# Performance work log

Measured on AMD Instinct MI355X. Metric: run time of the kernel, lower is better.

Reference implementation:

```python
import jax, jax.numpy as jnp
import numpy as np

B, S, E = 4, 2048, 2048
QH, KH = 16, 4
HD = E // QH            # 128 head dim
KVE = HD * KH           # 512 kv embed dim
LN_EPS = 1e-5


def act_quant(x):
    # BitNet 1.58: per-token 8-bit absmax activation quantization
    scale = 127.0 / jnp.clip(jnp.max(jnp.abs(x), axis=-1, keepdims=True), 1e-5)
    return jnp.clip(jnp.round(x * scale), -128.0, 127.0) / scale


def weight_quant(w):
    # BitNet 1.58: ternary {-1,0,1} weight quantization via mean-abs scale
    scale = 1.0 / jnp.clip(jnp.mean(jnp.abs(w)), 1e-5)
    return jnp.clip(jnp.round(w * scale), -1.0, 1.0) / scale


def bitlinear(x, w, b):
    # straight-through estimator form: quantized forward, identity backward
    xq = x + jax.lax.stop_gradient(act_quant(x) - x)
    wq = w + jax.lax.stop_gradient(weight_quant(w) - w)
    return xq @ wq.T + b


def setup_inputs() -> dict:
    ks = jax.random.split(jax.random.key(0), 16)
    w = lambda k, shp: jax.random.normal(k, shp, jnp.float32) * 0.02
    return {
        "query": jax.random.normal(ks[0], (B, S, E), jnp.float32),
        "key":   jax.random.normal(ks[1], (B, S, E), jnp.float32),
        "value": jax.random.normal(ks[2], (B, S, E), jnp.float32),
        "Wq": w(ks[3], (E, E)),   "bq": jnp.zeros((E,),   jnp.float32),
        "Wk": w(ks[4], (KVE, E)), "bk": jnp.zeros((KVE,), jnp.float32),
        "Wv": w(ks[5], (KVE, E)), "bv": jnp.zeros((KVE,), jnp.float32),
        "Wo": w(ks[6], (E, KVE)), "bo": jnp.zeros((E,),   jnp.float32),
        "gamma": jnp.ones((KVE,), jnp.float32),
        "beta":  jnp.zeros((KVE,), jnp.float32),
    }


def reference(query, key, value, Wq, bq, Wk, bk, Wv, bv, Wo, bo, gamma, beta):
    q = bitlinear(query, Wq, bq)   # [B,N,E]
    k = bitlinear(key,   Wk, bk)   # [B,S,KVE]
    v = bitlinear(value, Wv, bv)   # [B,S,KVE]
    b_, n = q.shape[0], q.shape[1]
    s = k.shape[1]
    q = q.reshape(b_, n, QH, HD)
    k = k.reshape(b_, s, KH, HD)
    v = v.reshape(b_, s, KH, HD)
    scale = float(HD) ** 0.5
    # b h n d with query heads split into (kv_head, group); group axis is SUMMED
    # (faithful to the source einsum 'b g h n d, b h s d -> b h n s')
    qh = (q / scale).transpose(0, 2, 1, 3).reshape(b_, KH, QH // KH, n, HD)
    kh = k.transpose(0, 2, 1, 3)   # [B,KH,S,HD]
    vh = v.transpose(0, 2, 1, 3)   # [B,KH,S,HD]
    sim = jnp.einsum('bhgnd,bhsd->bhns', qh, kh)
    mask = jnp.tril(jnp.ones((n, s), dtype=bool))
    sim = jnp.where(mask, sim, jnp.finfo(sim.dtype).min)
    # note: source divides by scale twice (q/scale then sim/scale)
    attn = jax.nn.softmax(sim / scale, axis=-1)
    out = jnp.einsum('bhns,bhsd->bhnd', attn, vh)
    x = out.transpose(0, 2, 1, 3).reshape(b_, n, KVE)
    mu = jnp.mean(x, axis=-1, keepdims=True)
    var = jnp.var(x, axis=-1, keepdims=True)
    x = (x - mu) / jnp.sqrt(var + LN_EPS) * gamma + beta
    return bitlinear(x, Wo, bo)
```

## Files before the change

### kernel.cpp

```cpp
#include <hip/hip_runtime.h>
#include <hip/hip_fp16.h>

typedef _Float16 f16;
typedef __attribute__((ext_vector_type(8))) _Float16 f16x8;
typedef __attribute__((ext_vector_type(4))) _Float16 f16x4;
typedef __attribute__((ext_vector_type(2))) _Float16 f16x2;
typedef __attribute__((ext_vector_type(4))) float f32x4;

#define AS1(p) ((__attribute__((address_space(1))) char*)(p))
#define AS3(p) ((__attribute__((address_space(3))) char*)(p))

static __device__ __forceinline__ float wave_red_sum(float v) {
#pragma unroll
  for (int m = 1; m < 64; m <<= 1) v += __shfl_xor(v, m);
  return v;
}
static __device__ __forceinline__ float wave_red_max(float v) {
#pragma unroll
  for (int m = 1; m < 64; m <<= 1) v = fmaxf(v, __shfl_xor(v, m));
  return v;
}

__global__ __launch_bounds__(256) void absum_partial(
    const float* __restrict__ Wq, const float* __restrict__ Wk,
    const float* __restrict__ Wv, const float* __restrict__ Wo,
    float* __restrict__ partial) {
  const int w = blockIdx.x >> 8;
  const int lb = blockIdx.x & 255;
  const float* W = (w == 0) ? Wq : (w == 1) ? Wk : (w == 2) ? Wv : Wo;
  const int per_block = (w == 0) ? (4194304 >> 8) : (1048576 >> 8);
  const float* base = W + (size_t)lb * per_block;
  float s = 0.f;
  for (int i = threadIdx.x * 4; i < per_block; i += 256 * 4) {
    float4 v = *(const float4*)(base + i);
    s += fabsf(v.x) + fabsf(v.y) + fabsf(v.z) + fabsf(v.w);
  }
  s = wave_red_sum(s);
  __shared__ float red[4];
  const int wave = threadIdx.x >> 6, lane = threadIdx.x & 63;
  if (lane == 0) red[wave] = s;
  __syncthreads();
  if (threadIdx.x == 0) partial[blockIdx.x] = red[0] + red[1] + red[2] + red[3];
}

__global__ __launch_bounds__(256) void absum_final(const float* __restrict__ partial,
                                                   float* __restrict__ scales) {
  const int wave = threadIdx.x >> 6, lane = threadIdx.x & 63;
  const float* p = partial + wave * 256;
  float s = p[lane] + p[lane + 64] + p[lane + 128] + p[lane + 192];
  s = wave_red_sum(s);
  if (lane == 0) {
    const float cnt = (wave == 0) ? 4194304.f : 1048576.f;
    const float mean = s / cnt;
    const float mul = 1.0f / fmaxf(mean, 1e-5f);
    scales[wave] = mul;
    scales[4 + wave] = 1.0f / mul;
  }
}

__global__ __launch_bounds__(256) void quant_w_ternary(const float* __restrict__ W,
                                                       f16* __restrict__ W8,
                                                       const float* __restrict__ scales,
                                                       int widx, int n) {
  const float mul = scales[widx];
  const int i = (blockIdx.x * 256 + threadIdx.x) * 4;
  if (i >= n) return;
  float4 v = *(const float4*)(W + i);
  f16x4 o;
  o[0] = (f16)fminf(fmaxf(rintf(v.x * mul), -1.f), 1.f);
  o[1] = (f16)fminf(fmaxf(rintf(v.y * mul), -1.f), 1.f);
  o[2] = (f16)fminf(fmaxf(rintf(v.z * mul), -1.f), 1.f);
  o[3] = (f16)fminf(fmaxf(rintf(v.w * mul), -1.f), 1.f);
  *(f16x4*)(W8 + i) = o;
}

__global__ __launch_bounds__(256) void quant_wq_eff(const float* __restrict__ Wq,
                                                    f16* __restrict__ We,
                                                    const float* __restrict__ scales) {
  const float mul = scales[0];
  const int idx = (blockIdx.x * 256 + threadIdx.x) * 4;
  const int j = idx >> 11, e = idx & 2047;
  const int h = j >> 7, d = j & 127;
  float a0 = 0, a1 = 0, a2 = 0, a3 = 0;
#pragma unroll
  for (int g = 0; g < 4; g++) {
    const float* src = Wq + (size_t)((h * 4 + g) * 128 + d) * 2048 + e;
    float4 v = *(const float4*)src;
    a0 += fminf(fmaxf(rintf(v.x * mul), -1.f), 1.f);
    a1 += fminf(fmaxf(rintf(v.y * mul), -1.f), 1.f);
    a2 += fminf(fmaxf(rintf(v.z * mul), -1.f), 1.f);
    a3 += fminf(fmaxf(rintf(v.w * mul), -1.f), 1.f);
  }
  f16x4 o; o[0] = (f16)a0; o[1] = (f16)a1; o[2] = (f16)a2; o[3] = (f16)a3;
  *(f16x4*)(We + idx) = o;
}

__global__ void bq_eff_kernel(const float* __restrict__ bq, float* __restrict__ be) {
  const int j = blockIdx.x * 256 + threadIdx.x;
  if (j >= 512) return;
  const int h = j >> 7, d = j & 127;
  float s = 0.f;
#pragma unroll
  for (int g = 0; g < 4; g++) s += bq[(h * 4 + g) * 128 + d];
  be[j] = s;
}

__global__ __launch_bounds__(256) void quant_act3(
    const float* __restrict__ Xq, const float* __restrict__ Xk, const float* __restrict__ Xv,
    f16* __restrict__ Aq, f16* __restrict__ Ak, f16* __restrict__ Av,
    float* __restrict__ deq3) {
  const int which = blockIdx.y;
  const float* X = which == 0 ? Xq : which == 1 ? Xk : Xv;
  f16* Q = which == 0 ? Aq : which == 1 ? Ak : Av;
  float* deq = deq3 + which * 8192;
  const size_t tok = blockIdx.x;
  const float* x = X + tok * 2048;
  const int t = threadIdx.x;
  float4 v0 = *(const float4*)(x + t * 8);
  float4 v1 = *(const float4*)(x + t * 8 + 4);
  float amax = fmaxf(fmaxf(fmaxf(fabsf(v0.x), fabsf(v0.y)), fmaxf(fabsf(v0.z), fabsf(v0.w))),
                     fmaxf(fmaxf(fabsf(v1.x), fabsf(v1.y)), fmaxf(fabsf(v1.z), fabsf(v1.w))));
  amax = wave_red_max(amax);
  __shared__ float red[4];
  const int wave = t >> 6, lane = t & 63;
  if (lane == 0) red[wave] = amax;
  __syncthreads();
  amax = fmaxf(fmaxf(red[0], red[1]), fmaxf(red[2], red[3]));
  const float scale = 127.0f / fmaxf(amax, 1e-5f);
  f16x8 q;
  q[0] = (f16)fminf(fmaxf(rintf(v0.x * scale), -128.f), 127.f);
  q[1] = (f16)fminf(fmaxf(rintf(v0.y * scale), -128.f), 127.f);
  q[2] = (f16)fminf(fmaxf(rintf(v0.z * scale), -128.f), 127.f);
  q[3] = (f16)fminf(fmaxf(rintf(v0.w * scale), -128.f), 127.f);
  q[4] = (f16)fminf(fmaxf(rintf(v1.x * scale), -128.f), 127.f);
  q[5] = (f16)fminf(fmaxf(rintf(v1.y * scale), -128.f), 127.f);
  q[6] = (f16)fminf(fmaxf(rintf(v1.z * scale), -128.f), 127.f);
  q[7] = (f16)fminf(fmaxf(rintf(v1.w * scale), -128.f), 127.f);
  *(f16x8*)(Q + tok * 2048 + t * 8) = q;
  if (t == 0) deq[tok] = 1.0f / scale;
}

template <typename OutT>
static __device__ __forceinline__ void gemm_core(
    const f16* __restrict__ A, const f16* __restrict__ W,
    const float* __restrict__ deqA, const float dW,
    const float* __restrict__ bias, OutT* __restrict__ C,
    const int N, const int K, const float out_scale, const int bm, const int bn,
    f16* __restrict__ As, f16* __restrict__ Bs) {
  const int t = threadIdx.x;
  const int wave = t >> 6, lane = t & 63;
  const int lg = lane >> 4, ln = lane & 15;
  const int wr = (wave >> 1) * 64, wc = (wave & 1) * 64;
  f32x4 acc[4][4] = {};
  const f16* gA = A + (size_t)(bm * 128 + (t >> 2)) * K + (t & 3) * 8;
  const f16* gB = W + (size_t)(bn * 128 + (t >> 2)) * K + (t & 3) * 8;
  const int wb = wave * 1024;

  for (int k0 = 0; k0 < K; k0 += 32) {
    __builtin_amdgcn_global_load_lds(AS1(gA + k0), AS3((char*)As + wb), 16, 0, 0);
    __builtin_amdgcn_global_load_lds(AS1(gA + (size_t)64 * K + k0), AS3((char*)As + 4096 + wb), 16, 0, 0);
    __builtin_amdgcn_global_load_lds(AS1(gB + k0), AS3((char*)Bs + wb), 16, 0, 0);
    __builtin_amdgcn_global_load_lds(AS1(gB + (size_t)64 * K + k0), AS3((char*)Bs + 4096 + wb), 16, 0, 0);
    __syncthreads();
    f16x8 af[4], bf[4];
#pragma unroll
    for (int fr = 0; fr < 4; fr++) af[fr] = *(const f16x8*)(As + (wr + fr * 16 + ln) * 32 + lg * 8);
#pragma unroll
    for (int fc = 0; fc < 4; fc++) bf[fc] = *(const f16x8*)(Bs + (wc + fc * 16 + ln) * 32 + lg * 8);
    __builtin_amdgcn_s_setprio(1);
#pragma unroll
    for (int fr = 0; fr < 4; fr++)
#pragma unroll
      for (int fc = 0; fc < 4; fc++)
        acc[fr][fc] = __builtin_amdgcn_mfma_f32_16x16x32_f16(af[fr], bf[fc], acc[fr][fc], 0, 0, 0);
    __builtin_amdgcn_s_setprio(0);
    __syncthreads();
  }
#pragma unroll
  for (int fr = 0; fr < 4; fr++) {
#pragma unroll
    for (int r = 0; r < 4; r++) {
      const int grow = bm * 128 + wr + fr * 16 + lg * 4 + r;
      const float dA = deqA[grow] * dW;
#pragma unroll
      for (int fc = 0; fc < 4; fc++) {
        const int gcol = bn * 128 + wc + fc * 16 + ln;
        const float y = (acc[fr][fc][r] * dA + bias[gcol]) * out_scale;
        C[(size_t)grow * N + gcol] = (OutT)y;
      }
    }
  }
}

__global__ __launch_bounds__(256) void gemm_qkv(
    const f16* __restrict__ Aq, const f16* __restrict__ Ak, const f16* __restrict__ Av,
    const f16* __restrict__ Wqe, const f16* __restrict__ Wk8, const f16* __restrict__ Wv8,
    const float* __restrict__ deq3, const float* __restrict__ scales,
    const float* __restrict__ bqe, const float* __restrict__ bk, const float* __restrict__ bv,
    f16* __restrict__ Cq, f16* __restrict__ Ck, f16* __restrict__ Cv) {
  __shared__ f16 As[128 * 32];
  __shared__ f16 Bs[128 * 32];
  const int orig = blockIdx.x + (blockIdx.y << 2) + (blockIdx.z << 8);
  const int wk = ((orig & 7) * 96) + (orig >> 3);
  const int z = wk >> 8, rem = wk & 255, bm = rem >> 2, bn = rem & 3;
  const f16* A = z == 0 ? Aq : z == 1 ? Ak : Av;
  const f16* W = z == 0 ? Wqe : z == 1 ? Wk8 : Wv8;
  const float* bias = z == 0 ? bqe : z == 1 ? bk : bv;
  f16* C = z == 0 ? Cq : z == 1 ? Ck : Cv;
  gemm_core<f16>(A, W, deq3 + z * 8192, scales[4 + z], bias, C,
                 512, 2048, z == 0 ? (1.0f / 128.0f) : 1.0f, bm, bn, As, Bs);
}

__global__ __launch_bounds__(256) void gemm_o(
    const f16* __restrict__ A, const f16* __restrict__ W,
    const float* __restrict__ deqA, const float* __restrict__ scales,
    const float* __restrict__ bias, float* __restrict__ C) {
  __shared__ f16 As[128 * 32];
  __shared__ f16 Bs[128 * 32];
  const int orig = blockIdx.x + (blockIdx.y << 4);
  const int wk = ((orig & 7) * 128) + (orig >> 3);
  const int bm = wk >> 4, bn = wk & 15;
  gemm_core<float>(A, W, deqA, scales[7], bias, C, 2048, 512, 1.0f, bm, bn, As, Bs);
}

static __device__ __forceinline__ void stage_k(char* ksb, const f16* src, int wave) {
#pragma unroll
  for (int i = 0; i < 4; i++)
    __builtin_amdgcn_global_load_lds(AS1(src + (size_t)i * 16 * 512),
                                     AS3(ksb + i * 4096 + wave * 1024), 16, 0, 0);
}

static __device__ __forceinline__ void write_v(f16* vsb, int vsp, int vdp,
                                               f16x8 va0, f16x8 va1, f16x8 vb0, f16x8 vb1) {
#pragma unroll
  for (int j = 0; j < 8; j++) {
    const int d0 = vdp + j;
    const int m0 = ((d0 ^ (d0 >> 4)) & 7) << 3;
    f16x2 p0; p0[0] = va0[j]; p0[1] = vb0[j];
    *(f16x2*)(vsb + d0 * 64 + (vsp ^ m0)) = p0;
    const int d1 = vdp + 8 + j;
    const int m1 = ((d1 ^ (d1 >> 4)) & 7) << 3;
    f16x2 p1; p1[0] = va1[j]; p1[1] = vb1[j];
    *(f16x2*)(vsb + d1 * 64 + (vsp ^ m1)) = p1;
  }
}

__global__ __launch_bounds__(256) void attn_kernel(
    const f16* __restrict__ Qs, const f16* __restrict__ Kq, const f16* __restrict__ Vq,
    float* __restrict__ X) {
  __shared__ f16 Ks[2][64 * 128];
  __shared__ f16 Vs[2][128 * 64];
  __shared__ f16 Ps[4][16 * 72];
  const int pr = blockIdx.x, bh = blockIdx.y;
  const int b = bh >> 2, h = bh & 3;
  const int t = threadIdx.x, wave = t >> 6, lane = t & 63;
  const int lg = lane >> 4, ln = lane & 15;
  const size_t base = (size_t)b * 2048 * 512 + h * 128;

  const int krow16 = wave * 4 + (lane >> 4);
  const int kcol = ((lane & 15) * 8) ^ ((krow16 & 7) << 3);
  const f16* gK0 = Kq + base + (size_t)krow16 * 512 + kcol;
  const int vsp = (t >> 3) * 2, vdp = (t & 7) * 16;
  const f16* gV0 = Vq + base + (size_t)vsp * 512 + vdp;

  for (int pass = 0; pass < 2; ++pass) {
    const int qt = pass ? (31 - pr) : pr;
    const int nt = qt + 1;
    f16x8 qf[4];
    {
      const int qrow = qt * 64 + wave * 16 + ln;
      const f16* qp = Qs + base + (size_t)qrow * 512 + lg * 8;
#pragma unroll
      for (int ks = 0; ks < 4; ks++) qf[ks] = *(const f16x8*)(qp + ks * 32);
    }
    f32x4 o[8] = {};
    float m_r[4], l_r[4];
#pragma unroll
    for (int r = 0; r < 4; r++) { m_r[r] = -1e30f; l_r[r] = 0.f; }

    f16x8 va0, va1, vb0, vb1;
    stage_k((char*)&Ks[0][0], gK0, wave);
    {
      const f16* gv = gV0;
      va0 = *(const f16x8*)(gv);       va1 = *(const f16x8*)(gv + 8);
      vb0 = *(const f16x8*)(gv + 512); vb1 = *(const f16x8*)(gv + 520);
    }
    write_v(&Vs[0][0], vsp, vdp, va0, va1, vb0, vb1);
    __syncthreads();

    for (int ti = 0; ti < nt; ++ti) {
      const int buf = ti & 1, nbuf = buf ^ 1;
      const bool pf = (ti + 1 < nt);
      if (pf) {
        stage_k((char*)&Ks[nbuf][0], gK0 + (size_t)(ti + 1) * 64 * 512, wave);
        const f16* gv = gV0 + (size_t)(ti + 1) * 64 * 512;
        va0 = *(const f16x8*)(gv);       va1 = *(const f16x8*)(gv + 8);
        vb0 = *(const f16x8*)(gv + 512); vb1 = *(const f16x8*)(gv + 520);
      }
      const int s0 = ti * 64;
      f32x4 sacc[4] = {};
      __builtin_amdgcn_s_setprio(1);
#pragma unroll
      for (int ks = 0; ks < 4; ks++)
#pragma unroll
        for (int fc = 0; fc < 4; fc++) {
          const int row = fc * 16 + ln;
          f16x8 bf = *(const f16x8*)(&Ks[buf][row * 128 + ((ks * 32 + lg * 8) ^ ((ln & 7) << 3))]);
          sacc[fc] = __builtin_amdgcn_mfma_f32_16x16x32_f16(qf[ks], bf, sacc[fc], 0, 0, 0);
        }
      __builtin_amdgcn_s_setprio(0);
      if (ti == nt - 1) {
        const int rbase = qt * 64 + wave * 16 + lg * 4;
#pragma unroll
        for (int fc = 0; fc < 4; fc++) {
          const int col = s0 + fc * 16 + ln;
#pragma unroll
          for (int r = 0; r < 4; r++)
            if (col > rbase + r) sacc[fc][r] = -1e30f;
        }
      }
      float tm[4];
#pragma unroll
      for (int r = 0; r < 4; r++)
        tm[r] = fmaxf(fmaxf(sacc[0][r], sacc[1][r]), fmaxf(sacc[2][r], sacc[3][r]));
#pragma unroll
      for (int r = 0; r < 4; r++) {
#pragma unroll
        for (int msk = 1; msk < 16; msk <<= 1) tm[r] = fmaxf(tm[r], __shfl_xor(tm[r], msk));
      }
      float al[4], ps[4];
#pragma unroll
      for (int r = 0; r < 4; r++) {
        const float mn = fmaxf(m_r[r], tm[r]);
        al[r] = __expf(m_r[r] - mn);
        m_r[r] = mn;
        ps[r] = 0.f;
      }
#pragma unroll
      for (int fc = 0; fc < 4; fc++)
#pragma unroll
        for (int r = 0; r < 4; r++) {
          const float p = __expf(sacc[fc][r] - m_r[r]);
          ps[r] += p;
          Ps[wave][(lg * 4 + r) * 72 + fc * 16 + ln] = (f16)p;
        }
#pragma unroll
      for (int r = 0; r < 4; r++) {
#pragma unroll
        for (int msk = 1; msk < 16; msk <<= 1) ps[r] += __shfl_xor(ps[r], msk);
        l_r[r] = l_r[r] * al[r] + ps[r];
      }
#pragma unroll
      for (int fc2 = 0; fc2 < 8; fc2++)
#pragma unroll
        for (int r = 0; r < 4; r++) o[fc2][r] *= al[r];
      __builtin_amdgcn_s_setprio(1);
#pragma unroll
      for (int ks2 = 0; ks2 < 2; ks2++) {
        f16x8 pa = *(const f16x8*)(&Ps[wave][ln * 72 + ks2 * 32 + lg * 8]);
#pragma unroll
        for (int fc2 = 0; fc2 < 8; fc2++) {
          const int d = fc2 * 16 + ln;
          f16x8 vbf = *(const f16x8*)(&Vs[buf][d * 64 +
                          ((ks2 * 32 + lg * 8) ^ (((ln ^ fc2) & 7) << 3))]);
          o[fc2] = __builtin_amdgcn_mfma_f32_16x16x32_f16(pa, vbf, o[fc2], 0, 0, 0);
        }
      }
      __builtin_amdgcn_s_setprio(0);
      if (pf) write_v(&Vs[nbuf][0], vsp, vdp, va0, va1, vb0, vb1);
      __syncthreads();
    }
    const int rbase = qt * 64 + wave * 16 + lg * 4;
#pragma unroll
    for (int r = 0; r < 4; r++) {
      const float inv = 1.0f / l_r[r];
      float* xp = X + ((size_t)b * 2048 + rbase + r) * 512 + h * 128 + ln;
#pragma unroll
      for (int fc2 = 0; fc2 < 8; fc2++) xp[fc2 * 16] = o[fc2][r] * inv;
    }
  }
}

__global__ __launch_bounds__(256) void ln_quant(const float* __restrict__ X,
                                                const float* __restrict__ gamma,
                                                const float* __restrict__ beta,
                                                f16* __restrict__ Q, float* __restrict__ deq) {
  const size_t tok = blockIdx.x;
  const int t = threadIdx.x;
  const float* x = X + tok * 512;
  float2 v = *(const float2*)(x + t * 2);
  float s = v.x + v.y, sq = v.x * v.x + v.y * v.y;
  s = wave_red_sum(s);
  sq = wave_red_sum(sq);
  __shared__ float rs[4], rq[4], rm[4];
  const int wave = t >> 6, lane = t & 63;
  if (lane == 0) { rs[wave] = s; rq[wave] = sq; }
  __syncthreads();
  s = rs[0] + rs[1] + rs[2] + rs[3];
  sq = rq[0] + rq[1] + rq[2] + rq[3];
  const float mean = s * (1.0f / 512.0f);
  const float var = sq * (1.0f / 512.0f) - mean * mean;
  const float inv = 1.0f / sqrtf(var + 1e-5f);
  float2 g = *(const float2*)(gamma + t * 2);
  float2 be = *(const float2*)(beta + t * 2);
  const float t0 = (v.x - mean) * inv * g.x + be.x;
  const float t1 = (v.y - mean) * inv * g.y + be.y;
  float amax = fmaxf(fabsf(t0), fabsf(t1));
  amax = wave_red_max(amax);
  if (lane == 0) rm[wave] = amax;
  __syncthreads();
  amax = fmaxf(fmaxf(rm[0], rm[1]), fmaxf(rm[2], rm[3]));
  const float scale = 127.0f / fmaxf(amax, 1e-5f);
  f16x2 q;
  q[0] = (f16)fminf(fmaxf(rintf(t0 * scale), -128.f), 127.f);
  q[1] = (f16)fminf(fmaxf(rintf(t1 * scale), -128.f), 127.f);
  *(f16x2*)(Q + tok * 512 + t * 2) = q;
  if (t == 0) deq[tok] = 1.0f / scale;
}

extern "C" void kernel_launch(void* const* d_in, const int* in_sizes, int n_in,
                              void* d_out, int out_size, void* d_ws, size_t ws_size,
                              hipStream_t stream) {
  const float* query = (const float*)d_in[0];
  const float* key   = (const float*)d_in[1];
  const float* value = (const float*)d_in[2];
  const float* Wq = (const float*)d_in[3];
  const float* bq = (const float*)d_in[4];
  const float* Wk = (const float*)d_in[5];
  const float* bk = (const float*)d_in[6];
  const float* Wv = (const float*)d_in[7];
  const float* bv = (const float*)d_in[8];
  const float* Wo = (const float*)d_in[9];
  const float* bo = (const float*)d_in[10];
  const float* gamma = (const float*)d_in[11];
  const float* beta  = (const float*)d_in[12];

  char* ws = (char*)d_ws;
  size_t off = 0;
  auto alloc = [&](size_t bytes) {
    char* p = ws + off;
    off = (off + bytes + 255) & ~(size_t)255;
    return p;
  };
  float* partial = (float*)alloc(1024 * 4);
  float* scales  = (float*)alloc(8 * 4);
  float* bqe     = (float*)alloc(512 * 4);
  f16* Wqe = (f16*)alloc((size_t)512 * 2048 * 2);
  f16* Wk8 = (f16*)alloc((size_t)512 * 2048 * 2);
  f16* Wv8 = (f16*)alloc((size_t)512 * 2048 * 2);
  f16* Wo8 = (f16*)alloc((size_t)2048 * 512 * 2);
  f16* a8v = (f16*)alloc((size_t)8192 * 2048 * 2);
  float* deq3 = (float*)alloc(3 * 8192 * 4);
  float* deqO = (float*)alloc(8192 * 4);
  f16* qs = (f16*)alloc((size_t)8192 * 512 * 2);
  f16* kq = (f16*)alloc((size_t)8192 * 512 * 2);
  f16* vq = (f16*)alloc((size_t)8192 * 512 * 2);
  float* x = (float*)alloc((size_t)8192 * 512 * 4);
  f16* a8o = (f16*)alloc((size_t)8192 * 512 * 2);
  (void)ws_size; (void)in_sizes; (void)n_in; (void)out_size;

  f16* a8q = (f16*)d_out;
  f16* a8k = (f16*)d_out + (size_t)8192 * 2048;

  absum_partial<<<1024, 256, 0, stream>>>(Wq, Wk, Wv, Wo, partial);
  absum_final<<<1, 256, 0, stream>>>(partial, scales);
  quant_wq_eff<<<1024, 256, 0, stream>>>(Wq, Wqe, scales);
  bq_eff_kernel<<<2, 256, 0, stream>>>(bq, bqe);
  quant_w_ternary<<<1024, 256, 0, stream>>>(Wk, Wk8, scales, 1, 1048576);
  quant_w_ternary<<<1024, 256, 0, stream>>>(Wv, Wv8, scales, 2, 1048576);
  quant_w_ternary<<<1024, 256, 0, stream>>>(Wo, Wo8, scales, 3, 1048576);

  quant_act3<<<dim3(8192, 3), 256, 0, stream>>>(query, key, value, a8q, a8k, a8v, deq3);
  gemm_qkv<<<dim3(4, 64, 3), 256, 0, stream>>>(a8q, a8k, a8v, Wqe, Wk8, Wv8, deq3, scales,
                                               bqe, bk, bv, qs, kq, vq);

  attn_kernel<<<dim3(16, 16), 256, 0, stream>>>(qs, kq, vq, x);

  ln_quant<<<8192, 256, 0, stream>>>(x, gamma, beta, a8o, deqO);
  gemm_o<<<dim3(16, 64), 256, 0, stream>>>(a8o, Wo8, deqO, scales, bo, (float*)d_out);
}
```

Measured before the change: 484.4 us.

## Switch bitlinear GEMMs to int8 MFMA with double-buffered swizzled LDS

```diff
diff --git a/kernel.cpp b/kernel.cpp
--- a/kernel.cpp
+++ b/kernel.cpp
@@ -6,6 +6,7 @@
 typedef __attribute__((ext_vector_type(4))) _Float16 f16x4;
 typedef __attribute__((ext_vector_type(2))) _Float16 f16x2;
 typedef __attribute__((ext_vector_type(4))) float f32x4;
+typedef __attribute__((ext_vector_type(4))) int i32x4;
 
 #define AS1(p) ((__attribute__((address_space(1))) char*)(p))
 #define AS3(p) ((__attribute__((address_space(3))) char*)(p))
@@ -19,6 +20,9 @@
 #pragma unroll
   for (int m = 1; m < 64; m <<= 1) v = fmaxf(v, __shfl_xor(v, m));
   return v;
+}
+static __device__ __forceinline__ int pack4(int q0, int q1, int q2, int q3) {
+  return (q0 & 255) | ((q1 & 255) << 8) | ((q2 & 255) << 16) | ((q3 & 255) << 24);
 }
 
 __global__ __launch_bounds__(256) void absum_partial(
@@ -58,24 +62,33 @@
   }
 }
 
-__global__ __launch_bounds__(256) void quant_w_ternary(const float* __restrict__ W,
-                                                       f16* __restrict__ W8,
-                                                       const float* __restrict__ scales,
-                                                       int widx, int n) {
-  const float mul = scales[widx];
-  const int i = (blockIdx.x * 256 + threadIdx.x) * 4;
-  if (i >= n) return;
-  float4 v = *(const float4*)(W + i);
-  f16x4 o;
-  o[0] = (f16)fminf(fmaxf(rintf(v.x * mul), -1.f), 1.f);
-  o[1] = (f16)fminf(fmaxf(rintf(v.y * mul), -1.f), 1.f);
-  o[2] = (f16)fminf(fmaxf(rintf(v.z * mul), -1.f), 1.f);
-  o[3] = (f16)fminf(fmaxf(rintf(v.w * mul), -1.f), 1.f);
-  *(f16x4*)(W8 + i) = o;
+__global__ __launch_bounds__(256) void quant_w3(
+    const float* __restrict__ Wk, const float* __restrict__ Wv, const float* __restrict__ Wo,
+    char* __restrict__ Ok, char* __restrict__ Ov, char* __restrict__ Oo,
+    const float* __restrict__ scales) {
+  const int z = blockIdx.y;
+  const float* W = z == 0 ? Wk : z == 1 ? Wv : Wo;
+  char* O = z == 0 ? Ok : z == 1 ? Ov : Oo;
+  const float mul = scales[1 + z];
+  const int i = (blockIdx.x * 256 + threadIdx.x) * 8;
+  float4 a = *(const float4*)(W + i);
+  float4 b = *(const float4*)(W + i + 4);
+  const int q0 = (int)fminf(fmaxf(rintf(a.x * mul), -1.f), 1.f);
+  const int q1 = (int)fminf(fmaxf(rintf(a.y * mul), -1.f), 1.f);
+  const int q2 = (int)fminf(fmaxf(rintf(a.z * mul), -1.f), 1.f);
+  const int q3 = (int)fminf(fmaxf(rintf(a.w * mul), -1.f), 1.f);
+  const int q4 = (int)fminf(fmaxf(rintf(b.x * mul), -1.f), 1.f);
+  const int q5 = (int)fminf(fmaxf(rintf(b.y * mul), -1.f), 1.f);
+  const int q6 = (int)fminf(fmaxf(rintf(b.z * mul), -1.f), 1.f);
+  const int q7 = (int)fminf(fmaxf(rintf(b.w * mul), -1.f), 1.f);
+  int2 p;
+  p.x = pack4(q0, q1, q2, q3);
+  p.y = pack4(q4, q5, q6, q7);
+  *(int2*)(O + i) = p;
 }
 
 __global__ __launch_bounds__(256) void quant_wq_eff(const float* __restrict__ Wq,
-                                                    f16* __restrict__ We,
+                                                    char* __restrict__ We,
                                                     const float* __restrict__ scales) {
   const float mul = scales[0];
   const int idx = (blockIdx.x * 256 + threadIdx.x) * 4;
@@ -91,8 +104,7 @@
     a2 += fminf(fmaxf(rintf(v.z * mul), -1.f), 1.f);
     a3 += fminf(fmaxf(rintf(v.w * mul), -1.f), 1.f);
   }
-  f16x4 o; o[0] = (f16)a0; o[1] = (f16)a1; o[2] = (f16)a2; o[3] = (f16)a3;
-  *(f16x4*)(We + idx) = o;
+  *(int*)(We + idx) = pack4((int)a0, (int)a1, (int)a2, (int)a3);
 }
 
 __global__ void bq_eff_kernel(const float* __restrict__ bq, float* __restrict__ be) {
@@ -107,11 +119,11 @@
 
 __global__ __launch_bounds__(256) void quant_act3(
     const float* __restrict__ Xq, const float* __restrict__ Xk, const float* __restrict__ Xv,
-    f16* __restrict__ Aq, f16* __restrict__ Ak, f16* __restrict__ Av,
+    char* __restrict__ Aq, char* __restrict__ Ak, char* __restrict__ Av,
     float* __restrict__ deq3) {
   const int which = blockIdx.y;
   const float* X = which == 0 ? Xq : which == 1 ? Xk : Xv;
-  f16* Q = which == 0 ? Aq : which == 1 ? Ak : Av;
+  char* Q = which == 0 ? Aq : which == 1 ? Ak : Av;
   float* deq = deq3 + which * 8192;
   const size_t tok = blockIdx.x;
   const float* x = X + tok * 2048;
@@ -127,54 +139,69 @@
   __syncthreads();
   amax = fmaxf(fmaxf(red[0], red[1]), fmaxf(red[2], red[3]));
   const float scale = 127.0f / fmaxf(amax, 1e-5f);
-  f16x8 q;
-  q[0] = (f16)fminf(fmaxf(rintf(v0.x * scale), -128.f), 127.f);
-  q[1] = (f16)fminf(fmaxf(rintf(v0.y * scale), -128.f), 127.f);
-  q[2] = (f16)fminf(fmaxf(rintf(v0.z * scale), -128.f), 127.f);
-  q[3] = (f16)fminf(fmaxf(rintf(v0.w * scale), -128.f), 127.f);
-  q[4] = (f16)fminf(fmaxf(rintf(v1.x * scale), -128.f), 127.f);
-  q[5] = (f16)fminf(fmaxf(rintf(v1.y * scale), -128.f), 127.f);
-  q[6] = (f16)fminf(fmaxf(rintf(v1.z * scale), -128.f), 127.f);
-  q[7] = (f16)fminf(fmaxf(rintf(v1.w * scale), -128.f), 127.f);
-  *(f16x8*)(Q + tok * 2048 + t * 8) = q;
+  const int q0 = (int)fminf(fmaxf(rintf(v0.x * scale), -128.f), 127.f);
+  const int q1 = (int)fminf(fmaxf(rintf(v0.y * scale), -128.f), 127.f);
+  const int q2 = (int)fminf(fmaxf(rintf(v0.z * scale), -128.f), 127.f);
+  const int q3 = (int)fminf(fmaxf(rintf(v0.w * scale), -128.f), 127.f);
+  const int q4 = (int)fminf(fmaxf(rintf(v1.x * scale), -128.f), 127.f);
+  const int q5 = (int)fminf(fmaxf(rintf(v1.y * scale), -128.f), 127.f);
+  const int q6 = (int)fminf(fmaxf(rintf(v1.z * scale), -128.f), 127.f);
+  const int q7 = (int)fminf(fmaxf(rintf(v1.w * scale), -128.f), 127.f);
+  int2 p;
+  p.x = pack4(q0, q1, q2, q3);
+  p.y = pack4(q4, q5, q6, q7);
+  *(int2*)(Q + tok * 2048 + t * 8) = p;
   if (t == 0) deq[tok] = 1.0f / scale;
 }
 
+static __device__ __forceinline__ void stage_i8(const char* src, char* dst, int wave, int K) {
+  __builtin_amdgcn_global_load_lds(AS1(src), AS3(dst + wave * 1024), 16, 0, 0);
+  __builtin_amdgcn_global_load_lds(AS1(src + (size_t)64 * K), AS3(dst + 4096 + wave * 1024), 16, 0, 0);
+}
+
 template <typename OutT>
-static __device__ __forceinline__ void gemm_core(
-    const f16* __restrict__ A, const f16* __restrict__ W,
+static __device__ __forceinline__ void gemm_core_i8(
+    const char* __restrict__ A, const char* __restrict__ W,
     const float* __restrict__ deqA, const float dW,
     const float* __restrict__ bias, OutT* __restrict__ C,
     const int N, const int K, const float out_scale, const int bm, const int bn,
-    f16* __restrict__ As, f16* __restrict__ Bs) {
+    char* As, char* Bs) {
   const int t = threadIdx.x;
   const int wave = t >> 6, lane = t & 63;
   const int lg = lane >> 4, ln = lane & 15;
   const int wr = (wave >> 1) * 64, wc = (wave & 1) * 64;
-  f32x4 acc[4][4] = {};
-  const f16* gA = A + (size_t)(bm * 128 + (t >> 2)) * K + (t & 3) * 8;
-  const f16* gB = W + (size_t)(bn * 128 + (t >> 2)) * K + (t & 3) * 8;
-  const int wb = wave * 1024;
-
-  for (int k0 = 0; k0 < K; k0 += 32) {
-    __builtin_amdgcn_global_load_lds(AS1(gA + k0), AS3((char*)As + wb), 16, 0, 0);
-    __builtin_amdgcn_global_load_lds(AS1(gA + (size_t)64 * K + k0), AS3((char*)As + 4096 + wb), 16, 0, 0);
-    __builtin_amdgcn_global_load_lds(AS1(gB + k0), AS3((char*)Bs + wb), 16, 0, 0);
-    __builtin_amdgcn_global_load_lds(AS1(gB + (size_t)64 * K + k0), AS3((char*)Bs + 4096 + wb), 16, 0, 0);
-    __syncthreads();
-    f16x8 af[4], bf[4];
-#pragma unroll
-    for (int fr = 0; fr < 4; fr++) af[fr] = *(const f16x8*)(As + (wr + fr * 16 + ln) * 32 + lg * 8);
-#pragma unroll
-    for (int fc = 0; fc < 4; fc++) bf[fc] = *(const f16x8*)(Bs + (wc + fc * 16 + ln) * 32 + lg * 8);
+  i32x4 acc[4][4] = {};
+  const int swS = ((t & 3) ^ ((t >> 3) & 3)) * 16;
+  const char* gA = A + (size_t)(bm * 128 + (t >> 2)) * K + swS;
+  const char* gB = W + (size_t)(bn * 128 + (t >> 2)) * K + swS;
+  const int swR = (lg ^ ((ln >> 1) & 3)) * 16;
+  const int NI = K >> 6;
+
+  stage_i8(gA, As, wave, K);
+  stage_i8(gB, Bs, wave, K);
+  __syncthreads();
+  int buf = 0;
+  for (int it = 0; it < NI; ++it) {
+    if (it + 1 < NI) {
+      stage_i8(gA + (it + 1) * 64, As + ((buf ^ 1) << 13), wave, K);
+      stage_i8(gB + (it + 1) * 64, Bs + ((buf ^ 1) << 13), wave, K);
+    }
+    i32x4 af[4], bf[4];
+#pragma unroll
+    for (int fr = 0; fr < 4; fr++)
+      af[fr] = *(const i32x4*)(As + (buf << 13) + (wr + fr * 16 + ln) * 64 + swR);
+#pragma unroll
+    for (int fc = 0; fc < 4; fc++)
+      bf[fc] = *(const i32x4*)(Bs + (buf << 13) + (wc + fc * 16 + ln) * 64 + swR);
     __builtin_amdgcn_s_setprio(1);
 #pragma unroll
     for (int fr = 0; fr < 4; fr++)
 #pragma unroll
       for (int fc = 0; fc < 4; fc++)
-        acc[fr][fc] = __builtin_amdgcn_mfma_f32_16x16x32_f16(af[fr], bf[fc], acc[fr][fc], 0, 0, 0);
+        acc[fr][fc] = __builtin_amdgcn_mfma_i32_16x16x64_i8(af[fr], bf[fc], acc[fr][fc], 0, 0, 0);
     __builtin_amdgcn_s_setprio(0);
     __syncthreads();
+    buf ^= 1;
   }
 #pragma unroll
   for (int fr = 0; fr < 4; fr++) {
@@ -185,42 +212,42 @@
 #pragma unroll
       for (int fc = 0; fc < 4; fc++) {
         const int gcol = bn * 128 + wc + fc * 16 + ln;
-        const float y = (acc[fr][fc][r] * dA + bias[gcol]) * out_scale;
-        C[(size_t)grow * N + gcol] = (OutT)y;
+        C[(size_t)grow * N + gcol] = (OutT)(((float)acc[fr][fc][r] * dA + bias[gcol]) * out_scale);
       }
     }
   }
 }
 
 __global__ __launch_bounds__(256) void gemm_qkv(
-    const f16* __restrict__ Aq, const f16* __restrict__ Ak, const f16* __restrict__ Av,
-    const f16* __restrict__ Wqe, const f16* __restrict__ Wk8, const f16* __restrict__ Wv8,
+    const char* __restrict__ Aq, const char* __restrict__ Ak, const char* __restrict__ Av,
+    const char* __restrict__ Wqe, const char* __restrict__ Wk8, const char* __restrict__ Wv8,
     const float* __restrict__ deq3, const float* __restrict__ scales,
     const float* __restrict__ bqe, const float* __restrict__ bk, const float* __restrict__ bv,
     f16* __restrict__ Cq, f16* __restrict__ Ck, f16* __restrict__ Cv) {
-  __shared__ f16 As[128 * 32];
-  __shared__ f16 Bs[128 * 32];
+  __shared__ __align__(16) char As[2][8192];
+  __shared__ __align__(16) char Bs[2][8192];
   const int orig = blockIdx.x + (blockIdx.y << 2) + (blockIdx.z << 8);
   const int wk = ((orig & 7) * 96) + (orig >> 3);
   const int z = wk >> 8, rem = wk & 255, bm = rem >> 2, bn = rem & 3;
-  const f16* A = z == 0 ? Aq : z == 1 ? Ak : Av;
-  const f16* W = z == 0 ? Wqe : z == 1 ? Wk8 : Wv8;
+  const char* A = z == 0 ? Aq : z == 1 ? Ak : Av;
+  const char* W = z == 0 ? Wqe : z == 1 ? Wk8 : Wv8;
   const float* bias = z == 0 ? bqe : z == 1 ? bk : bv;
   f16* C = z == 0 ? Cq : z == 1 ? Ck : Cv;
-  gemm_core<f16>(A, W, deq3 + z * 8192, scales[4 + z], bias, C,
-                 512, 2048, z == 0 ? (1.0f / 128.0f) : 1.0f, bm, bn, As, Bs);
+  gemm_core_i8<f16>(A, W, deq3 + z * 8192, scales[4 + z], bias, C,
+                    512, 2048, z == 0 ? (1.0f / 128.0f) : 1.0f, bm, bn, &As[0][0], &Bs[0][0]);
 }
 
 __global__ __launch_bounds__(256) void gemm_o(
-    const f16* __restrict__ A, const f16* __restrict__ W,
+    const char* __restrict__ A, const char* __restrict__ W,
     const float* __restrict__ deqA, const float* __restrict__ scales,
     const float* __restrict__ bias, float* __restrict__ C) {
-  __shared__ f16 As[128 * 32];
-  __shared__ f16 Bs[128 * 32];
+  __shared__ __align__(16) char As[2][8192];
+  __shared__ __align__(16) char Bs[2][8192];
   const int orig = blockIdx.x + (blockIdx.y << 4);
   const int wk = ((orig & 7) * 128) + (orig >> 3);
   const int bm = wk >> 4, bn = wk & 15;
-  gemm_core<float>(A, W, deqA, scales[7], bias, C, 2048, 512, 1.0f, bm, bn, As, Bs);
+  gemm_core_i8<float>(A, W, deqA, scales[7], bias, C, 2048, 512, 1.0f, bm, bn,
+                      &As[0][0], &Bs[0][0]);
 }
 
 static __device__ __forceinline__ void stage_k(char* ksb, const f16* src, int wave) {
@@ -384,7 +411,7 @@
 __global__ __launch_bounds__(256) void ln_quant(const float* __restrict__ X,
                                                 const float* __restrict__ gamma,
                                                 const float* __restrict__ beta,
-                                                f16* __restrict__ Q, float* __restrict__ deq) {
+                                                char* __restrict__ Q, float* __restrict__ deq) {
   const size_t tok = blockIdx.x;
   const int t = threadIdx.x;
   const float* x = X + tok * 512;
@@ -411,10 +438,9 @@
   __syncthreads();
   amax = fmaxf(fmaxf(rm[0], rm[1]), fmaxf(rm[2], rm[3]));
   const float scale = 127.0f / fmaxf(amax, 1e-5f);
-  f16x2 q;
-  q[0] = (f16)fminf(fmaxf(rintf(t0 * scale), -128.f), 127.f);
-  q[1] = (f16)fminf(fmaxf(rintf(t1 * scale), -128.f), 127.f);
-  *(f16x2*)(Q + tok * 512 + t * 2) = q;
+  const int q0 = (int)fminf(fmaxf(rintf(t0 * scale), -128.f), 127.f);
+  const int q1 = (int)fminf(fmaxf(rintf(t1 * scale), -128.f), 127.f);
+  *(unsigned short*)(Q + tok * 512 + t * 2) = (unsigned short)((q0 & 255) | ((q1 & 255) << 8));
   if (t == 0) deq[tok] = 1.0f / scale;
 }
 
@@ -445,30 +471,28 @@
   float* partial = (float*)alloc(1024 * 4);
   float* scales  = (float*)alloc(8 * 4);
   float* bqe     = (float*)alloc(512 * 4);
-  f16* Wqe = (f16*)alloc((size_t)512 * 2048 * 2);
-  f16* Wk8 = (f16*)alloc((size_t)512 * 2048 * 2);
-  f16* Wv8 = (f16*)alloc((size_t)512 * 2048 * 2);
-  f16* Wo8 = (f16*)alloc((size_t)2048 * 512 * 2);
-  f16* a8v = (f16*)alloc((size_t)8192 * 2048 * 2);
+  char* Wqe = alloc((size_t)512 * 2048);
+  char* Wk8 = alloc((size_t)512 * 2048);
+  char* Wv8 = alloc((size_t)512 * 2048);
+  char* Wo8 = alloc((size_t)2048 * 512);
+  char* a8v = alloc((size_t)8192 * 2048);
   float* deq3 = (float*)alloc(3 * 8192 * 4);
   float* deqO = (float*)alloc(8192 * 4);
   f16* qs = (f16*)alloc((size_t)8192 * 512 * 2);
   f16* kq = (f16*)alloc((size_t)8192 * 512 * 2);
   f16* vq = (f16*)alloc((size_t)8192 * 512 * 2);
   float* x = (float*)alloc((size_t)8192 * 512 * 4);
-  f16* a8o = (f16*)alloc((size_t)8192 * 512 * 2);
+  char* a8o = alloc((size_t)8192 * 512);
   (void)ws_size; (void)in_sizes; (void)n_in; (void)out_size;
 
-  f16* a8q = (f16*)d_out;
-  f16* a8k = (f16*)d_out + (size_t)8192 * 2048;
+  char* a8q = (char*)d_out;
+  char* a8k = (char*)d_out + (size_t)8192 * 2048;
 
   absum_partial<<<1024, 256, 0, stream>>>(Wq, Wk, Wv, Wo, partial);
   absum_final<<<1, 256, 0, stream>>>(partial, scales);
   quant_wq_eff<<<1024, 256, 0, stream>>>(Wq, Wqe, scales);
   bq_eff_kernel<<<2, 256, 0, stream>>>(bq, bqe);
-  quant_w_ternary<<<1024, 256, 0, stream>>>(Wk, Wk8, scales, 1, 1048576);
-  quant_w_ternary<<<1024, 256, 0, stream>>>(Wv, Wv8, scales, 2, 1048576);
-  quant_w_ternary<<<1024, 256, 0, stream>>>(Wo, Wo8, scales, 3, 1048576);
+  quant_w3<<<dim3(512, 3), 256, 0, stream>>>(Wk, Wv, Wo, Wk8, Wv8, Wo8, scales);
 
   quant_act3<<<dim3(8192, 3), 256, 0, stream>>>(query, key, value, a8q, a8k, a8v, deq3);
   gemm_qkv<<<dim3(4, 64, 3), 256, 0, stream>>>(a8q, a8k, a8v, Wqe, Wk8, Wv8, deq3, scales,
```

After: 408.7 us. -15.6%, faster.
